# Optimization experiments

Measured on AMD Instinct MI355X. Metric: run time of the kernel, lower is better.

The kernel has to match this reference:

```python
import jax, jax.numpy as jnp
import numpy as np

N = 50000      # nodes
E = 800000     # edges (avg degree 16)
H = 128        # hidden_dim
ED = 8         # edge_dim
TD = 64        # time_dim
EIN = 2 * H + 1 + ED + TD  # 329, phi_e input dim


def _linear_params(key, fan_in, fan_out):
    kw, kb = jax.random.split(key)
    s = 1.0 / np.sqrt(fan_in)
    W = jax.random.uniform(kw, (fan_in, fan_out), minval=-s, maxval=s, dtype=jnp.float32)
    b = jax.random.uniform(kb, (fan_out,), minval=-s, maxval=s, dtype=jnp.float32)
    return W, b


def setup_inputs() -> dict:
    key = jax.random.key(0)
    ks = jax.random.split(key, 12)
    h = jax.random.normal(ks[0], (N, H), dtype=jnp.float32)
    x = jax.random.normal(ks[1], (N, 3), dtype=jnp.float32)
    edge_attr = jax.random.normal(ks[2], (E, ED), dtype=jnp.float32)
    t_emb = jax.random.normal(ks[3], (N, TD), dtype=jnp.float32)
    edge_index = jax.random.randint(ks[4], (2, E), 0, N, dtype=jnp.int32)
    We1_w, We1_b = _linear_params(ks[5], EIN, H)
    We2_w, We2_b = _linear_params(ks[6], H, H)
    Watt_w, Watt_b = _linear_params(ks[7], H, 1)
    Wx1_w, Wx1_b = _linear_params(ks[8], H, H)
    Wx2_w, Wx2_b = _linear_params(ks[9], H, 1)
    Wh1_w, Wh1_b = _linear_params(ks[10], 2 * H, H)
    Wh2_w, Wh2_b = _linear_params(ks[11], H, H)
    return dict(h=h, x=x, edge_attr=edge_attr, t_emb=t_emb,
                We1_w=We1_w, We1_b=We1_b, We2_w=We2_w, We2_b=We2_b,
                Watt_w=Watt_w, Watt_b=Watt_b,
                Wx1_w=Wx1_w, Wx1_b=Wx1_b, Wx2_w=Wx2_w, Wx2_b=Wx2_b,
                Wh1_w=Wh1_w, Wh1_b=Wh1_b, Wh2_w=Wh2_w, Wh2_b=Wh2_b,
                edge_index=edge_index)


def reference(h, x, edge_attr, t_emb,
              We1_w, We1_b, We2_w, We2_b,
              Watt_w, Watt_b,
              Wx1_w, Wx1_b, Wx2_w, Wx2_b,
              Wh1_w, Wh1_b, Wh2_w, Wh2_b,
              edge_index):
    src, dst = edge_index[0], edge_index[1]
    diff = x[src] - x[dst]                                   # (E, 3)
    dist_sq = jnp.sum(diff * diff, axis=-1, keepdims=True)   # (E, 1)
    # m_ij = phi_e(h_i || h_j || ||x_i - x_j||^2 || edge_attr || t_emb)
    msg_in = jnp.concatenate([h[src], h[dst], dist_sq, edge_attr, t_emb[src]], axis=-1)  # (E, EIN)
    m = jax.nn.silu(msg_in @ We1_w + We1_b) @ We2_w + We2_b  # (E, H)
    # attention gate
    att = jax.nn.sigmoid(m @ Watt_w + Watt_b)                # (E, 1)
    m = att * m
    # equivariant coordinate update
    coord_w = jnp.tanh(jax.nn.silu(m @ Wx1_w + Wx1_b) @ Wx2_w + Wx2_b)  # (E, 1)
    coord_shift = diff * coord_w                             # (E, 3)
    coord_agg = jax.ops.segment_sum(coord_shift, dst, num_segments=N)   # (N, 3)
    deg = jax.ops.segment_sum(jnp.ones((dst.shape[0], 1), dtype=x.dtype), dst, num_segments=N)
    x_out = x + coord_agg / (deg + 1.0)
    # invariant feature update with residual
    msg_agg = jax.ops.segment_sum(m, dst, num_segments=N)    # (N, H)
    h_in = jnp.concatenate([h, msg_agg], axis=-1)            # (N, 2H)
    h_out = h + (jax.nn.silu(h_in @ Wh1_w + Wh1_b) @ Wh2_w + Wh2_b)
    return (h_out, x_out)
```

## Files before the change

kernel.cpp:

```cpp
#include <hip/hip_runtime.h>
#include <hip/hip_fp16.h>

typedef unsigned short u16;
typedef unsigned int u32;
typedef __attribute__((ext_vector_type(8))) short short8;
typedef __attribute__((ext_vector_type(4))) float f32x4;

#define NN 50000
#define EE 800000
#define SCAN_B 49

__device__ __forceinline__ float bf2f(u16 u){ union{u32 i; float f;} v; v.i=((u32)u)<<16; return v.f; }
__device__ __forceinline__ u16 f2bf(float f){ union{float f; u32 i;} v; v.f=f; u32 b=v.i; b += 0x7FFFu + ((b>>16)&1u); return (u16)(b>>16); }
__device__ __forceinline__ float sigmoidf_(float x){ return 1.0f/(1.0f+__expf(-x)); }

__device__ __forceinline__ void cvt8(uint4 q, float* f){
  f[0]=bf2f((u16)(q.x&0xFFFF)); f[1]=bf2f((u16)(q.x>>16));
  f[2]=bf2f((u16)(q.y&0xFFFF)); f[3]=bf2f((u16)(q.y>>16));
  f[4]=bf2f((u16)(q.z&0xFFFF)); f[5]=bf2f((u16)(q.z>>16));
  f[6]=bf2f((u16)(q.w&0xFFFF)); f[7]=bf2f((u16)(q.w>>16));
}
__device__ __forceinline__ uint4 pack8(const float* f){
  uint4 q;
  q.x=(u32)f2bf(f[0])|((u32)f2bf(f[1])<<16);
  q.y=(u32)f2bf(f[2])|((u32)f2bf(f[3])<<16);
  q.z=(u32)f2bf(f[4])|((u32)f2bf(f[5])<<16);
  q.w=(u32)f2bf(f[6])|((u32)f2bf(f[7])<<16);
  return q;
}

__device__ __forceinline__ float h2f(u16 u){ __half h; *reinterpret_cast<u16*>(&h)=u; return (float)h; }
__device__ __forceinline__ u32 f2h2pack(float lo, float hi){
  __half2 h2 = __floats2half2_rn(lo, hi);
  return *reinterpret_cast<u32*>(&h2);
}
__device__ __forceinline__ void atomic_pk_add_f16(u16* addr, u32 data){
  asm volatile("global_atomic_pk_add_f16 %0, %1, off" :: "v"(addr), "v"(data) : "memory");
}

template<int FP32> struct IO;
template<> struct IO<0> {
  static __device__ __forceinline__ float ld(const void* p, int i){ return bf2f(((const u16*)p)[i]); }
  static __device__ __forceinline__ void ld8(const void* p, int i, float* f){
    cvt8(*(const uint4*)((const u16*)p + i), f);
  }
  static __device__ __forceinline__ void st(void* p, int i, float v){ ((u16*)p)[i] = f2bf(v); }
};
template<> struct IO<1> {
  static __device__ __forceinline__ float ld(const void* p, int i){ return ((const float*)p)[i]; }
  static __device__ __forceinline__ void ld8(const void* p, int i, float* f){
    f32x4 a = *(const f32x4*)((const float*)p + i);
    f32x4 b = *(const f32x4*)((const float*)p + i + 4);
    f[0]=a[0]; f[1]=a[1]; f[2]=a[2]; f[3]=a[3];
    f[4]=b[0]; f[5]=b[1]; f[6]=b[2]; f[7]=b[3];
  }
  static __device__ __forceinline__ void st(void* p, int i, float v){ ((float*)p)[i] = v; }
};

__device__ __forceinline__ void atomic_add_bf16pair(u32* addr, float lo, float hi){
  u32 old = *addr, assumed;
  do {
    assumed = old;
    float flo = bf2f((u16)(assumed & 0xFFFFu)) + lo;
    float fhi = bf2f((u16)(assumed >> 16)) + hi;
    u32 newv = (u32)f2bf(flo) | ((u32)f2bf(fhi) << 16);
    if (newv == assumed) return;
    old = atomicCAS(addr, assumed, newv);
  } while (old != assumed);
}

__global__ void k_probe(const u16* __restrict__ hraw, int* __restrict__ flag){
  if (threadIdx.x==0 && blockIdx.x==0){
    float mx = 0.f; int zc = 0;
    for (int i = 0; i < 256; i += 2){
      u16 u = hraw[i];
      if (u == 0) zc++;
      float v = fabsf(bf2f(u));
      mx = fmaxf(mx, v);
    }
    flag[0] = (mx > 1e3f || zc > 32) ? 1 : 0;
  }
}

__global__ __launch_bounds__(256) void k_hist(const int* __restrict__ eidx, int* __restrict__ cnt){
  int e = blockIdx.x*256 + threadIdx.x;
  if (e < EE) atomicAdd(&cnt[eidx[EE+e]], 1);
}
__global__ __launch_bounds__(1024) void k_scanA(const int* __restrict__ cnt,
                                               int* __restrict__ rowoff, int* __restrict__ bsum){
  __shared__ int s[1024];
  int t = threadIdx.x, b = blockIdx.x, i = b*1024 + t;
  int v = (i < NN) ? cnt[i] : 0;
  s[t] = v; __syncthreads();
  #pragma unroll
  for (int off=1; off<1024; off<<=1){
    int add = (t>=off) ? s[t-off] : 0;
    __syncthreads();
    s[t] += add;
    __syncthreads();
  }
  rowoff[i+1] = s[t];
  if (t==1023) bsum[b] = s[t];
}
__global__ void k_scanB(int* __restrict__ bsum){
  if (threadIdx.x==0 && blockIdx.x==0){
    int acc=0;
    for (int b=0;b<SCAN_B;b++){ int v=bsum[b]; bsum[b]=acc; acc+=v; }
  }
}
__global__ __launch_bounds__(1024) void k_scanC(int* __restrict__ rowoff, int* __restrict__ cur,
                                               const int* __restrict__ bsum){
  int t = threadIdx.x, b = blockIdx.x, i = b*1024 + t;
  int v = rowoff[i+1] + bsum[b];
  rowoff[i+1] = v;
  if (i < NN-1) cur[i+1] = v;
  if (i==0){ rowoff[0]=0; cur[0]=0; }
}
__global__ __launch_bounds__(256) void k_scatter(const int* __restrict__ eidx,
                                                 int* __restrict__ cur, int* __restrict__ perm){
  int e = blockIdx.x*256 + threadIdx.x;
  if (e < EE){
    int p = atomicAdd(&cur[eidx[EE+e]], 1);
    perm[p] = e;
  }
}

template<int FP32>
__global__ __launch_bounds__(256) void k_prep(
    const int* __restrict__ flag,
    const void* __restrict__ We1, const void* __restrict__ We2,
    const void* __restrict__ Wx1, const void* __restrict__ Wh1,
    const void* __restrict__ Wh2,
    u16* __restrict__ WprojT, u16* __restrict__ We2T, u16* __restrict__ Wx1T,
    u16* __restrict__ Wh1T, u16* __restrict__ Wh2T, u16* __restrict__ Wrk9T)
{
  if (flag[0] != FP32) return;
  int i = blockIdx.x*256 + threadIdx.x;
  if (i < 49152){
    int n = i/192, k = i%192; float v;
    if (n < 128) v = (k<128) ? IO<FP32>::ld(We1, k*128+n) : IO<FP32>::ld(We1, (265+k-128)*128+n);
    else         v = (k<128) ? IO<FP32>::ld(We1, (128+k)*128+(n-128)) : 0.f;
    WprojT[i] = f2bf(v);
  } else if (i < 65536){
    int j=i-49152; int n=j/128, k=j%128; We2T[j] = f2bf(IO<FP32>::ld(We2, k*128+n));
  } else if (i < 81920){
    int j=i-65536; int n=j/128, k=j%128; Wx1T[j] = f2bf(IO<FP32>::ld(Wx1, k*128+n));
  } else if (i < 114688){
    int j=i-81920; int n=j/256, k=j%256; Wh1T[j] = f2bf(IO<FP32>::ld(Wh1, k*128+n));
  } else if (i < 131072){
    int j=i-114688; int n=j/128, k=j%128; Wh2T[j] = f2bf(IO<FP32>::ld(Wh2, k*128+n));
  } else if (i < 135168){
    int j=i-131072; int n=j/32, k=j%32;
    float v = (k<=8) ? IO<FP32>::ld(We1, (256+k)*128+n) : 0.f;
    Wrk9T[j] = f2bf(v);
  }
}

template<int FP32, int WP2>
__global__ __launch_bounds__(256) void k_proj(
    const int* __restrict__ flag,
    const void* __restrict__ h, const void* __restrict__ temb,
    const u16* __restrict__ WprojT, const void* __restrict__ We1b,
    u16* __restrict__ P13, u16* __restrict__ P2)
{
  if (flag[0] != FP32) return;
  constexpr int NT = WP2 ? 16 : 8;
  __shared__ __align__(16) u16 s_a[64][200];
  int tid = threadIdx.x; int nbase = blockIdx.x*64;
  {
    u32* p = (u32*)&s_a[0][0];
    for (int i = tid; i < 6400; i += 256) p[i] = 0u;
  }
  __syncthreads();
  {
    int r = tid>>2, p = tid&3; int node = nbase + r;
    if (node < NN){
      #pragma unroll
      for (int c=0;c<6;c++){
        int col = p*48 + c*8;
        float f[8];
        if (col<128) IO<FP32>::ld8(h, node*128 + col, f);
        else         IO<FP32>::ld8(temb, node*64 + (col-128), f);
        *(uint4*)&s_a[r][col] = pack8(f);
      }
    }
  }
  __syncthreads();
  int lane=tid&63, wid=tid>>6, quad=lane>>4, l15=lane&15, mb=wid*16;
  f32x4 acc[NT];
  #pragma unroll
  for (int nt=0;nt<NT;nt++) acc[nt]=(f32x4){0.f,0.f,0.f,0.f};
  #pragma unroll
  for (int ks=0;ks<6;ks++){
    short8 af = *(const short8*)&s_a[mb+l15][ks*32+quad*8];
    #pragma unroll
    for (int nt=0;nt<NT;nt++){
      short8 bfr = *(const short8*)(WprojT + (nt*16+l15)*192 + ks*32+quad*8);
      acc[nt] = __builtin_amdgcn_mfma_f32_16x16x32_bf16(af, bfr, acc[nt], 0,0,0);
    }
  }
  #pragma unroll
  for (int r=0;r<4;r++){
    int node = nbase + mb + quad*4 + r;
    if (node < NN){
      #pragma unroll
      for (int nt=0;nt<NT;nt++){
        int colg = nt*16 + l15;
        float v = acc[nt][r];
        if (colg < 128) P13[node*128+colg] = f2bf(v + IO<FP32>::ld(We1b, colg));
        else if (WP2)   P2[node*128+(colg-128)] = f2bf(v);
      }
    }
  }
}

template<int FP32, int TIERA>
__global__ __launch_bounds__(256, 6) void k_edge(
    const int* __restrict__ flag,
    const void* __restrict__ x, const void* __restrict__ ea,
    const void* __restrict__ We1, const void* __restrict__ h,
    const void* __restrict__ We2b, const void* __restrict__ Watt, const void* __restrict__ Wattb,
    const void* __restrict__ Wx1b, const void* __restrict__ Wx2, const void* __restrict__ Wx2b,
    const int* __restrict__ eidx, const int* __restrict__ perm,
    const u16* __restrict__ P13, const u16* __restrict__ P2,
    const u16* __restrict__ WprojT, const u16* __restrict__ Wrk9T,
    const u16* __restrict__ We2T, const u16* __restrict__ Wx1T,
    u16* __restrict__ msgh, u16* __restrict__ msgb, float* __restrict__ cagg)
{
  if (flag[0] != FP32) return;
  __shared__ int s_dst[64];
  __shared__ float s_dif[64][3];
  __shared__ __align__(16) u16 s_hid[64][136];
  __shared__ __align__(16) u16 s_att[TIERA?64:1][40];
  __shared__ __align__(16) u16 s_m[TIERA?1:64][136];
  __shared__ __align__(16) u16 s_hd[TIERA?1:64][136];
  int tid = threadIdx.x;
  int ebase = blockIdx.x*64;
  {
    int el = tid>>2, p = tid&3;
    int e = TIERA ? perm[ebase+el] : (ebase+el);
    int srcI = eidx[e], dstI = eidx[EE+e];
    float d0 = IO<FP32>::ld(x, srcI*3+0) - IO<FP32>::ld(x, dstI*3+0);
    float d1 = IO<FP32>::ld(x, srcI*3+1) - IO<FP32>::ld(x, dstI*3+1);
    float d2 = IO<FP32>::ld(x, srcI*3+2) - IO<FP32>::ld(x, dstI*3+2);
    float dsq = d0*d0 + d1*d1 + d2*d2;
    if (p==0){ s_dst[el]=dstI; s_dif[el][0]=d0; s_dif[el][1]=d1; s_dif[el][2]=d2; }
    if constexpr (TIERA){
      if (p < 2){
        float eav[8]; IO<FP32>::ld8(ea, e*8, eav);
        float f9[8];
        if (p==0){ f9[0]=dsq; for (int t=0;t<7;t++) f9[1+t]=eav[t]; }
        else { f9[0]=eav[7]; for (int t=1;t<8;t++) f9[t]=0.f; }
        *(uint4*)&s_att[el][p*8] = pack8(f9);
      } else {
        *(uint4*)&s_att[el][p*8] = make_uint4(0,0,0,0);
      }
      const u16* p13r = P13 + srcI*128;
      const u16* p2r  = P2  + dstI*128;
      #pragma unroll
      for (int c=0;c<4;c++){
        int col = p*32 + c*8;
        float fa[8], fb[8];
        cvt8(*(const uint4*)(p13r+col), fa);
        cvt8(*(const uint4*)(p2r+col),  fb);
        #pragma unroll
        for (int i2=0;i2<8;i2++) fa[i2] += fb[i2];
        *(uint4*)&s_hid[el][col] = pack8(fa);
      }
    } else {
      float eav[8]; IO<FP32>::ld8(ea, e*8, eav);
      const u16* p13r = P13 + srcI*128;
      #pragma unroll
      for (int c=0;c<4;c++){
        int col = p*32 + c*8;
        float fw[8], pre[8];
        cvt8(*(const uint4*)(p13r+col), pre);
        IO<FP32>::ld8(We1, 256*128 + col, fw);
        #pragma unroll
        for (int i2=0;i2<8;i2++) pre[i2] += dsq*fw[i2];
        #pragma unroll
        for (int t=0;t<8;t++){
          IO<FP32>::ld8(We1, (257+t)*128 + col, fw);
          #pragma unroll
          for (int i2=0;i2<8;i2++) pre[i2] += eav[t]*fw[i2];
        }
        *(uint4*)&s_hid[el][col] = pack8(pre);
        float hd[8]; IO<FP32>::ld8(h, dstI*128 + col, hd);
        *(uint4*)&s_hd[el][col] = pack8(hd);
      }
    }
  }
  int lane=tid&63, wid=tid>>6, quad=lane>>4, l15=lane&15, mb=wid*16;
  if constexpr (TIERA){
    f32x4 acc9[8];
    #pragma unroll
    for (int nt=0;nt<8;nt++) acc9[nt]=(f32x4){0.f,0.f,0.f,0.f};
    short8 a9 = *(const short8*)&s_att[mb+l15][quad*8];
    #pragma unroll
    for (int nt=0;nt<8;nt++){
      short8 bfr = *(const short8*)(Wrk9T + (nt*16+l15)*32 + quad*8);
      acc9[nt] = __builtin_amdgcn_mfma_f32_16x16x32_bf16(a9, bfr, acc9[nt], 0,0,0);
    }
    #pragma unroll
    for (int r=0;r<4;r++){
      int row = mb + quad*4 + r;
      #pragma unroll
      for (int nt=0;nt<8;nt++){
        int col = nt*16+l15;
        float u = bf2f(s_hid[row][col]) + acc9[nt][r];
        u = u*sigmoidf_(u);
        s_hid[row][col] = f2bf(u);
      }
    }
  } else {
    f32x4 accg[8];
    #pragma unroll
    for (int nt=0;nt<8;nt++) accg[nt]=(f32x4){0.f,0.f,0.f,0.f};
    #pragma unroll
    for (int ks=0;ks<4;ks++){
      short8 af = *(const short8*)&s_hd[mb+l15][ks*32+quad*8];
      #pragma unroll
      for (int nt=0;nt<8;nt++){
        short8 bfr = *(const short8*)(WprojT + (128 + nt*16+l15)*192 + ks*32+quad*8);
        accg[nt] = __builtin_amdgcn_mfma_f32_16x16x32_bf16(af, bfr, accg[nt], 0,0,0);
      }
    }
    #pragma unroll
    for (int r=0;r<4;r++){
      int row = mb + quad*4 + r;
      #pragma unroll
      for (int nt=0;nt<8;nt++){
        int col = nt*16+l15;
        float u = bf2f(s_hid[row][col]) + accg[nt][r];
        u = u*sigmoidf_(u);
        s_hid[row][col] = f2bf(u);
      }
    }
  }
  f32x4 acc[8];
  #pragma unroll
  for (int nt=0;nt<8;nt++) acc[nt]=(f32x4){0.f,0.f,0.f,0.f};
  #pragma unroll
  for (int ks=0;ks<4;ks++){
    short8 af = *(const short8*)&s_hid[mb+l15][ks*32+quad*8];
    #pragma unroll
    for (int nt=0;nt<8;nt++){
      short8 bfr = *(const short8*)(We2T + (nt*16+l15)*128 + ks*32+quad*8);
      acc[nt] = __builtin_amdgcn_mfma_f32_16x16x32_bf16(af, bfr, acc[nt], 0,0,0);
    }
  }
  float b2v[8], wav[8];
  #pragma unroll
  for (int nt=0;nt<8;nt++){ b2v[nt]=IO<FP32>::ld(We2b, nt*16+l15); wav[nt]=IO<FP32>::ld(Watt, nt*16+l15); }
  float attb = IO<FP32>::ld(Wattb, 0);
  float mval[8][4]; float dotr[4];
  #pragma unroll
  for (int r=0;r<4;r++){
    float s=0.f;
    #pragma unroll
    for (int nt=0;nt<8;nt++){ mval[nt][r]=acc[nt][r]+b2v[nt]; s += mval[nt][r]*wav[nt]; }
    dotr[r]=s;
  }
  #pragma unroll
  for (int off=1;off<16;off<<=1){
    #pragma unroll
    for (int r=0;r<4;r++) dotr[r] += __shfl_xor(dotr[r], off);
  }
  if constexpr (TIERA){
    float racc[8];
    #pragma unroll
    for (int nt=0;nt<8;nt++) racc[nt]=0.f;
    #pragma unroll
    for (int r=0;r<4;r++){
      float att = sigmoidf_(dotr[r]+attb);
      int erow = mb + quad*4 + r;
      int dstN = s_dst[erow];
      bool emit = (r==3) || (s_dst[erow+1] != dstN);
      #pragma unroll
      for (int nt=0;nt<8;nt++){
        float v = mval[nt][r]*att;
        s_hid[erow][nt*16+l15] = f2bf(v);
        racc[nt] += v;
      }
      #pragma unroll
      for (int nt=0;nt<8;nt++){
        float part = __shfl_xor(racc[nt], 1);
        if (emit && ((l15 & 1) == 0)){
          atomic_pk_add_f16(msgh + dstN*128 + nt*16 + l15, f2h2pack(racc[nt], part));
        }
      }
      if (emit){
        #pragma unroll
        for (int nt=0;nt<8;nt++) racc[nt]=0.f;
      }
    }
  } else {
    #pragma unroll
    for (int r=0;r<4;r++){
      float att = sigmoidf_(dotr[r]+attb);
      int erow = mb + quad*4 + r;
      int dstN = s_dst[erow];
      #pragma unroll
      for (int nt=0;nt<8;nt++){
        float v = mval[nt][r]*att;
        mval[nt][r] = v;
        s_m[erow][nt*16+l15] = f2bf(v);
      }
      #pragma unroll
      for (int nt=0;nt<8;nt++){
        float part = __shfl_xor(mval[nt][r], 1);
        if ((l15 & 1) == 0){
          atomic_add_bf16pair((u32*)(msgb + dstN*128 + nt*16 + l15), mval[nt][r], part);
        }
      }
    }
  }
  f32x4 acc2[8];
  #pragma unroll
  for (int nt=0;nt<8;nt++) acc2[nt]=(f32x4){0.f,0.f,0.f,0.f};
  #pragma unroll
  for (int ks=0;ks<4;ks++){
    short8 af = TIERA ? *(const short8*)&s_hid[mb+l15][ks*32+quad*8]
                      : *(const short8*)&s_m[mb+l15][ks*32+quad*8];
    #pragma unroll
    for (int nt=0;nt<8;nt++){
      short8 bfr = *(const short8*)(Wx1T + (nt*16+l15)*128 + ks*32+quad*8);
      acc2[nt] = __builtin_amdgcn_mfma_f32_16x16x32_bf16(af, bfr, acc2[nt], 0,0,0);
    }
  }
  float bx1v[8], wx2v[8];
  #pragma unroll
  for (int nt=0;nt<8;nt++){ bx1v[nt]=IO<FP32>::ld(Wx1b, nt*16+l15); wx2v[nt]=IO<FP32>::ld(Wx2, nt*16+l15); }
  float bx2f = IO<FP32>::ld(Wx2b, 0);
  float dc[4];
  #pragma unroll
  for (int r=0;r<4;r++){
    float s=0.f;
    #pragma unroll
    for (int nt=0;nt<8;nt++){
      float u = acc2[nt][r] + bx1v[nt];
      u = u*sigmoidf_(u);
      s += u*wx2v[nt];
    }
    dc[r]=s;
  }
  #pragma unroll
  for (int off=1;off<16;off<<=1){
    #pragma unroll
    for (int r=0;r<4;r++) dc[r] += __shfl_xor(dc[r], off);
  }
  if constexpr (TIERA){
    if (l15==0){
      float c0=0.f, c1=0.f, c2=0.f;
      #pragma unroll
      for (int r=0;r<4;r++){
        float cw = tanhf(dc[r]+bx2f);
        int erow = mb + quad*4 + r;
        int dstN = s_dst[erow];
        c0 += s_dif[erow][0]*cw;
        c1 += s_dif[erow][1]*cw;
        c2 += s_dif[erow][2]*cw;
        bool emit = (r==3) || (s_dst[erow+1] != dstN);
        if (emit){
          atomicAdd(&cagg[dstN*4+0], c0);
          atomicAdd(&cagg[dstN*4+1], c1);
          atomicAdd(&cagg[dstN*4+2], c2);
          c0=c1=c2=0.f;
        }
      }
    }
  } else {
    #pragma unroll
    for (int r=0;r<4;r++){
      float cw = tanhf(dc[r]+bx2f);
      if (l15==0){
        int erow = mb + quad*4 + r;
        int dstN = s_dst[erow];
        atomicAdd(&cagg[dstN*4+0], s_dif[erow][0]*cw);
        atomicAdd(&cagg[dstN*4+1], s_dif[erow][1]*cw);
        atomicAdd(&cagg[dstN*4+2], s_dif[erow][2]*cw);
        atomicAdd(&cagg[dstN*4+3], 1.0f);
      }
    }
  }
}

template<int FP32, int MSGF>
__global__ __launch_bounds__(256) void k_node(
    const int* __restrict__ flag,
    const void* __restrict__ h, const void* __restrict__ x,
    const u16* __restrict__ msgh, const u16* __restrict__ msgb,
    const float* __restrict__ cagg, const int* __restrict__ rowoff,
    const u16* __restrict__ Wh1T, const void* __restrict__ Wh1b,
    const u16* __restrict__ Wh2T, const void* __restrict__ Wh2b,
    void* __restrict__ out)
{
  if (flag[0] != FP32) return;
  __shared__ __align__(16) u16 s_a[64][264];
  __shared__ __align__(16) u16 s_u[64][136];
  int tid = threadIdx.x; int nbase = blockIdx.x*64;
  {
    u32* p1 = (u32*)&s_a[0][0];
    for (int i = tid; i < 8448; i += 256) p1[i] = 0u;
  }
  __syncthreads();
  {
    int r = tid>>2, p = tid&3; int node = nbase + r;
    if (node < NN){
      #pragma unroll
      for (int c=0;c<8;c++){
        int col = p*64 + c*8;
        if (col < 128){
          float f[8]; IO<FP32>::ld8(h, node*128 + col, f);
          *(uint4*)&s_a[r][col] = pack8(f);
        } else if (MSGF){
          uint4 q = *(const uint4*)(msgh + node*128 + (col-128));
          float f[8];
          f[0]=h2f((u16)(q.x&0xFFFF)); f[1]=h2f((u16)(q.x>>16));
          f[2]=h2f((u16)(q.y&0xFFFF)); f[3]=h2f((u16)(q.y>>16));
          f[4]=h2f((u16)(q.z&0xFFFF)); f[5]=h2f((u16)(q.z>>16));
          f[6]=h2f((u16)(q.w&0xFFFF)); f[7]=h2f((u16)(q.w>>16));
          *(uint4*)&s_a[r][col] = pack8(f);
        } else {
          *(uint4*)&s_a[r][col] = *(const uint4*)(msgb + node*128 + (col-128));
        }
      }
    }
  }
  __syncthreads();
  int lane=tid&63, wid=tid>>6, quad=lane>>4, l15=lane&15, mb=wid*16;
  f32x4 acc[8];
  #pragma unroll
  for (int nt=0;nt<8;nt++) acc[nt]=(f32x4){0.f,0.f,0.f,0.f};
  #pragma unroll
  for (int ks=0;ks<8;ks++){
    short8 af = *(const short8*)&s_a[mb+l15][ks*32+quad*8];
    #pragma unroll
    for (int nt=0;nt<8;nt++){
      short8 bfr = *(const short8*)(Wh1T + (nt*16+l15)*256 + ks*32+quad*8);
      acc[nt] = __builtin_amdgcn_mfma_f32_16x16x32_bf16(af, bfr, acc[nt], 0,0,0);
    }
  }
  #pragma unroll
  for (int r=0;r<4;r++){
    int row = mb + quad*4 + r;
    #pragma unroll
    for (int nt=0;nt<8;nt++){
      int col = nt*16+l15;
      float u = acc[nt][r] + IO<FP32>::ld(Wh1b, col);
      u = u*sigmoidf_(u);
      s_u[row][col] = f2bf(u);
    }
  }
  f32x4 acc2[8];
  #pragma unroll
  for (int nt=0;nt<8;nt++) acc2[nt]=(f32x4){0.f,0.f,0.f,0.f};
  #pragma unroll
  for (int ks=0;ks<4;ks++){
    short8 af = *(const short8*)&s_u[mb+l15][ks*32+quad*8];
    #pragma unroll
    for (int nt=0;nt<8;nt++){
      short8 bfr = *(const short8*)(Wh2T + (nt*16+l15)*128 + ks*32+quad*8);
      acc2[nt] = __builtin_amdgcn_mfma_f32_16x16x32_bf16(af, bfr, acc2[nt], 0,0,0);
    }
  }
  #pragma unroll
  for (int r=0;r<4;r++){
    int node = nbase + mb + quad*4 + r;
    if (node < NN){
      #pragma unroll
      for (int nt=0;nt<8;nt++){
        int col = nt*16+l15;
        float v = IO<FP32>::ld(h, node*128+col) + acc2[nt][r] + IO<FP32>::ld(Wh2b, col);
        IO<FP32>::st(out, node*128+col, v);
      }
    }
  }
  if (tid < 64){
    int node = nbase + tid;
    if (node < NN){
      float deg = MSGF ? (float)(rowoff[node+1]-rowoff[node]) : cagg[node*4+3];
      float inv = 1.0f/(deg + 1.0f);
      #pragma unroll
      for (int c=0;c<3;c++){
        float v = IO<FP32>::ld(x, node*3+c) + cagg[node*4+c]*inv;
        IO<FP32>::st(out, NN*128 + node*3 + c, v);
      }
    }
  }
}

extern "C" void kernel_launch(void* const* d_in, const int* in_sizes, int n_in,
                              void* d_out, int out_size, void* d_ws, size_t ws_size,
                              hipStream_t stream) {
  const void* h     = d_in[0];
  const void* x     = d_in[1];
  const void* ea    = d_in[2];
  const void* temb  = d_in[3];
  const void* We1   = d_in[4];
  const void* We1b  = d_in[5];
  const void* We2   = d_in[6];
  const void* We2b  = d_in[7];
  const void* Watt  = d_in[8];
  const void* Wattb = d_in[9];
  const void* Wx1   = d_in[10];
  const void* Wx1b  = d_in[11];
  const void* Wx2   = d_in[12];
  const void* Wx2b  = d_in[13];
  const void* Wh1   = d_in[14];
  const void* Wh1b  = d_in[15];
  const void* Wh2   = d_in[16];
  const void* Wh2b  = d_in[17];
  const int* eidx   = (const int*)d_in[18];
  char* ws = (char*)d_ws;

  u16* WprojT = (u16*)(ws + 0);
  u16* We2T   = (u16*)(ws + 98304);
  u16* Wx1T   = (u16*)(ws + 131072);
  u16* Wh1T   = (u16*)(ws + 163840);
  u16* Wh2T   = (u16*)(ws + 229376);
  u16* Wrk9T  = (u16*)(ws + 262144);
  float* cagg = (float*)(ws + 270336);
  int* flag   = (int*)(ws + 1070336);
  bool tierA = (ws_size >= (size_t)39470592);
  u16* msgh   = (u16*)(ws + 1070592);
  u16* msgb   = (u16*)(ws + 1070592);
  u16* P2     = (u16*)(ws + 13870592);
  int* cnt    = (int*)(ws + 26670592);
  int* rowoff = (int*)(ws + 26871296);
  int* cur    = (int*)(ws + 27072512);
  int* bsum   = (int*)(ws + 27273216);
  int* perm   = (int*)(ws + 27273472);
  u16* P13    = (u16*)d_out;

  hipMemsetAsync(ws + 270336, 0, 13600256, stream);
  k_probe<<<1, 64, 0, stream>>>((const u16*)h, flag);
  if (tierA){
    hipMemsetAsync(cnt, 0, 200704, stream);
    k_hist<<<(EE+255)/256, 256, 0, stream>>>(eidx, cnt);
    k_scanA<<<SCAN_B, 1024, 0, stream>>>(cnt, rowoff, bsum);
    k_scanB<<<1, 64, 0, stream>>>(bsum);
    k_scanC<<<SCAN_B, 1024, 0, stream>>>(rowoff, cur, bsum);
    k_scatter<<<(EE+255)/256, 256, 0, stream>>>(eidx, cur, perm);
  }
  k_prep<0><<<528, 256, 0, stream>>>(flag, We1, We2, Wx1, Wh1, Wh2, WprojT, We2T, Wx1T, Wh1T, Wh2T, Wrk9T);
  k_prep<1><<<528, 256, 0, stream>>>(flag, We1, We2, Wx1, Wh1, Wh2, WprojT, We2T, Wx1T, Wh1T, Wh2T, Wrk9T);
  if (tierA){
    k_proj<0,1><<<(NN+63)/64, 256, 0, stream>>>(flag, h, temb, WprojT, We1b, P13, P2);
    k_proj<1,1><<<(NN+63)/64, 256, 0, stream>>>(flag, h, temb, WprojT, We1b, P13, P2);
    k_edge<0,1><<<EE/64, 256, 0, stream>>>(flag, x, ea, We1, h, We2b, Watt, Wattb, Wx1b, Wx2, Wx2b,
                                           eidx, perm, P13, P2, WprojT, Wrk9T, We2T, Wx1T, msgh, msgb, cagg);
    k_edge<1,1><<<EE/64, 256, 0, stream>>>(flag, x, ea, We1, h, We2b, Watt, Wattb, Wx1b, Wx2, Wx2b,
                                           eidx, perm, P13, P2, WprojT, Wrk9T, We2T, Wx1T, msgh, msgb, cagg);
    k_node<0,1><<<(NN+63)/64, 256, 0, stream>>>(flag, h, x, msgh, msgb, cagg, rowoff, Wh1T, Wh1b, Wh2T, Wh2b, d_out);
    k_node<1,1><<<(NN+63)/64, 256, 0, stream>>>(flag, h, x, msgh, msgb, cagg, rowoff, Wh1T, Wh1b, Wh2T, Wh2b, d_out);
  } else {
    k_proj<0,0><<<(NN+63)/64, 256, 0, stream>>>(flag, h, temb, WprojT, We1b, P13, P2);
    k_proj<1,0><<<(NN+63)/64, 256, 0, stream>>>(flag, h, temb, WprojT, We1b, P13, P2);
    k_edge<0,0><<<EE/64, 256, 0, stream>>>(flag, x, ea, We1, h, We2b, Watt, Wattb, Wx1b, Wx2, Wx2b,
                                           eidx, perm, P13, P2, WprojT, Wrk9T, We2T, Wx1T, msgh, msgb, cagg);
    k_edge<1,0><<<EE/64, 256, 0, stream>>>(flag, x, ea, We1, h, We2b, Watt, Wattb, Wx1b, Wx2, Wx2b,
                                           eidx, perm, P13, P2, WprojT, Wrk9T, We2T, Wx1T, msgh, msgb, cagg);
    k_node<0,0><<<(NN+63)/64, 256, 0, stream>>>(flag, h, x, msgh, msgb, cagg, rowoff, Wh1T, Wh1b, Wh2T, Wh2b, d_out);
    k_node<1,0><<<(NN+63)/64, 256, 0, stream>>>(flag, h, x, msgh, msgb, cagg, rowoff, Wh1T, Wh1b, Wh2T, Wh2b, d_out);
  }
}
```

Before: 945.9 us.

## Split edge kernel by tier and give each wave two 16-edge tiles

The templated edge kernel becomes two kernels. The tier-A kernel now handles 128 edges per block, with each wave computing two 16-row MFMA tiles that share every B-fragment load of the weight matrices. This halves the weight reads per edge and the block count, and the k-loops use unroll 1. It costs more registers and shared memory: launch bounds drop to 3 blocks per CU and each of two threads gathers half of a 128-column row.

```diff
diff --git a/kernel.cpp b/kernel.cpp
--- a/kernel.cpp
+++ b/kernel.cpp
@@ -214,166 +214,130 @@
   }
 }
 
-template<int FP32, int TIERA>
-__global__ __launch_bounds__(256, 6) void k_edge(
+template<int FP32>
+__global__ __launch_bounds__(256, 3) void k_edgeA(
     const int* __restrict__ flag,
     const void* __restrict__ x, const void* __restrict__ ea,
-    const void* __restrict__ We1, const void* __restrict__ h,
     const void* __restrict__ We2b, const void* __restrict__ Watt, const void* __restrict__ Wattb,
     const void* __restrict__ Wx1b, const void* __restrict__ Wx2, const void* __restrict__ Wx2b,
     const int* __restrict__ eidx, const int* __restrict__ perm,
     const u16* __restrict__ P13, const u16* __restrict__ P2,
-    const u16* __restrict__ WprojT, const u16* __restrict__ Wrk9T,
-    const u16* __restrict__ We2T, const u16* __restrict__ Wx1T,
-    u16* __restrict__ msgh, u16* __restrict__ msgb, float* __restrict__ cagg)
+    const u16* __restrict__ Wrk9T, const u16* __restrict__ We2T, const u16* __restrict__ Wx1T,
+    u16* __restrict__ msgh, float* __restrict__ cagg)
 {
   if (flag[0] != FP32) return;
-  __shared__ int s_dst[64];
-  __shared__ float s_dif[64][3];
-  __shared__ __align__(16) u16 s_hid[64][136];
-  __shared__ __align__(16) u16 s_att[TIERA?64:1][40];
-  __shared__ __align__(16) u16 s_m[TIERA?1:64][136];
-  __shared__ __align__(16) u16 s_hd[TIERA?1:64][136];
+  __shared__ int s_dst[128];
+  __shared__ float s_dif[128][3];
+  __shared__ __align__(16) u16 s_hid[128][136];
+  __shared__ __align__(16) u16 s_att[128][40];
   int tid = threadIdx.x;
-  int ebase = blockIdx.x*64;
+  int ebase = blockIdx.x*128;
   {
-    int el = tid>>2, p = tid&3;
-    int e = TIERA ? perm[ebase+el] : (ebase+el);
+    int el = tid>>1, p = tid&1;
+    int e = perm[ebase+el];
     int srcI = eidx[e], dstI = eidx[EE+e];
-    float d0 = IO<FP32>::ld(x, srcI*3+0) - IO<FP32>::ld(x, dstI*3+0);
-    float d1 = IO<FP32>::ld(x, srcI*3+1) - IO<FP32>::ld(x, dstI*3+1);
-    float d2 = IO<FP32>::ld(x, srcI*3+2) - IO<FP32>::ld(x, dstI*3+2);
-    float dsq = d0*d0 + d1*d1 + d2*d2;
-    if (p==0){ s_dst[el]=dstI; s_dif[el][0]=d0; s_dif[el][1]=d1; s_dif[el][2]=d2; }
-    if constexpr (TIERA){
-      if (p < 2){
-        float eav[8]; IO<FP32>::ld8(ea, e*8, eav);
-        float f9[8];
-        if (p==0){ f9[0]=dsq; for (int t=0;t<7;t++) f9[1+t]=eav[t]; }
-        else { f9[0]=eav[7]; for (int t=1;t<8;t++) f9[t]=0.f; }
-        *(uint4*)&s_att[el][p*8] = pack8(f9);
-      } else {
-        *(uint4*)&s_att[el][p*8] = make_uint4(0,0,0,0);
-      }
-      const u16* p13r = P13 + srcI*128;
-      const u16* p2r  = P2  + dstI*128;
-      #pragma unroll
-      for (int c=0;c<4;c++){
-        int col = p*32 + c*8;
-        float fa[8], fb[8];
-        cvt8(*(const uint4*)(p13r+col), fa);
-        cvt8(*(const uint4*)(p2r+col),  fb);
-        #pragma unroll
-        for (int i2=0;i2<8;i2++) fa[i2] += fb[i2];
-        *(uint4*)&s_hid[el][col] = pack8(fa);
-      }
+    if (p==0){
+      float d0 = IO<FP32>::ld(x, srcI*3+0) - IO<FP32>::ld(x, dstI*3+0);
+      float d1 = IO<FP32>::ld(x, srcI*3+1) - IO<FP32>::ld(x, dstI*3+1);
+      float d2 = IO<FP32>::ld(x, srcI*3+2) - IO<FP32>::ld(x, dstI*3+2);
+      float dsq = d0*d0 + d1*d1 + d2*d2;
+      s_dst[el]=dstI; s_dif[el][0]=d0; s_dif[el][1]=d1; s_dif[el][2]=d2;
+      float eav[8]; IO<FP32>::ld8(ea, e*8, eav);
+      float f9[8];
+      f9[0]=dsq; for (int t=0;t<7;t++) f9[1+t]=eav[t];
+      *(uint4*)&s_att[el][0] = pack8(f9);
+      f9[0]=eav[7]; for (int t=1;t<8;t++) f9[t]=0.f;
+      *(uint4*)&s_att[el][8] = pack8(f9);
     } else {
-      float eav[8]; IO<FP32>::ld8(ea, e*8, eav);
-      const u16* p13r = P13 + srcI*128;
-      #pragma unroll
-      for (int c=0;c<4;c++){
-        int col = p*32 + c*8;
-        float fw[8], pre[8];
-        cvt8(*(const uint4*)(p13r+col), pre);
-        IO<FP32>::ld8(We1, 256*128 + col, fw);
-        #pragma unroll
-        for (int i2=0;i2<8;i2++) pre[i2] += dsq*fw[i2];
-        #pragma unroll
-        for (int t=0;t<8;t++){
-          IO<FP32>::ld8(We1, (257+t)*128 + col, fw);
-          #pragma unroll
-          for (int i2=0;i2<8;i2++) pre[i2] += eav[t]*fw[i2];
-        }
-        *(uint4*)&s_hid[el][col] = pack8(pre);
-        float hd[8]; IO<FP32>::ld8(h, dstI*128 + col, hd);
-        *(uint4*)&s_hd[el][col] = pack8(hd);
-      }
-    }
-  }
-  int lane=tid&63, wid=tid>>6, quad=lane>>4, l15=lane&15, mb=wid*16;
-  if constexpr (TIERA){
-    f32x4 acc9[8];
-    #pragma unroll
-    for (int nt=0;nt<8;nt++) acc9[nt]=(f32x4){0.f,0.f,0.f,0.f};
-    short8 a9 = *(const short8*)&s_att[mb+l15][quad*8];
+      *(uint4*)&s_att[el][16] = make_uint4(0,0,0,0);
+      *(uint4*)&s_att[el][24] = make_uint4(0,0,0,0);
+    }
+    const u16* p13r = P13 + srcI*128;
+    const u16* p2r  = P2  + dstI*128;
+    #pragma unroll
+    for (int c=0;c<8;c++){
+      int col = p*64 + c*8;
+      float fa[8], fb[8];
+      cvt8(*(const uint4*)(p13r+col), fa);
+      cvt8(*(const uint4*)(p2r+col),  fb);
+      #pragma unroll
+      for (int i2=0;i2<8;i2++) fa[i2] += fb[i2];
+      *(uint4*)&s_hid[el][col] = pack8(fa);
+    }
+  }
+  int lane=tid&63, wid=tid>>6, quad=lane>>4, l15=lane&15;
+  int rb = wid*32;
+  f32x4 acc9[2][8];
+  #pragma unroll
+  for (int t=0;t<2;t++)
+    #pragma unroll
+    for (int nt=0;nt<8;nt++) acc9[t][nt]=(f32x4){0.f,0.f,0.f,0.f};
+  {
+    short8 a90 = *(const short8*)&s_att[rb+l15][quad*8];
+    short8 a91 = *(const short8*)&s_att[rb+16+l15][quad*8];
     #pragma unroll
     for (int nt=0;nt<8;nt++){
       short8 bfr = *(const short8*)(Wrk9T + (nt*16+l15)*32 + quad*8);
-      acc9[nt] = __builtin_amdgcn_mfma_f32_16x16x32_bf16(a9, bfr, acc9[nt], 0,0,0);
-    }
+      acc9[0][nt] = __builtin_amdgcn_mfma_f32_16x16x32_bf16(a90, bfr, acc9[0][nt], 0,0,0);
+      acc9[1][nt] = __builtin_amdgcn_mfma_f32_16x16x32_bf16(a91, bfr, acc9[1][nt], 0,0,0);
+    }
+  }
+  #pragma unroll
+  for (int t=0;t<2;t++){
     #pragma unroll
     for (int r=0;r<4;r++){
-      int row = mb + quad*4 + r;
+      int row = rb + t*16 + quad*4 + r;
       #pragma unroll
       for (int nt=0;nt<8;nt++){
         int col = nt*16+l15;
-        float u = bf2f(s_hid[row][col]) + acc9[nt][r];
+        float u = bf2f(s_hid[row][col]) + acc9[t][nt][r];
         u = u*sigmoidf_(u);
         s_hid[row][col] = f2bf(u);
       }
     }
-  } else {
-    f32x4 accg[8];
-    #pragma unroll
-    for (int nt=0;nt<8;nt++) accg[nt]=(f32x4){0.f,0.f,0.f,0.f};
-    #pragma unroll
-    for (int ks=0;ks<4;ks++){
-      short8 af = *(const short8*)&s_hd[mb+l15][ks*32+quad*8];
-      #pragma unroll
-      for (int nt=0;nt<8;nt++){
-        short8 bfr = *(const short8*)(WprojT + (128 + nt*16+l15)*192 + ks*32+quad*8);
-        accg[nt] = __builtin_amdgcn_mfma_f32_16x16x32_bf16(af, bfr, accg[nt], 0,0,0);
-      }
-    }
-    #pragma unroll
-    for (int r=0;r<4;r++){
-      int row = mb + quad*4 + r;
-      #pragma unroll
-      for (int nt=0;nt<8;nt++){
-        int col = nt*16+l15;
-        float u = bf2f(s_hid[row][col]) + accg[nt][r];
-        u = u*sigmoidf_(u);
-        s_hid[row][col] = f2bf(u);
-      }
-    }
-  }
-  f32x4 acc[8];
-  #pragma unroll
-  for (int nt=0;nt<8;nt++) acc[nt]=(f32x4){0.f,0.f,0.f,0.f};
-  #pragma unroll
+  }
+  f32x4 acc[2][8];
+  #pragma unroll
+  for (int t=0;t<2;t++)
+    #pragma unroll
+    for (int nt=0;nt<8;nt++) acc[t][nt]=(f32x4){0.f,0.f,0.f,0.f};
+  #pragma unroll 1
   for (int ks=0;ks<4;ks++){
-    short8 af = *(const short8*)&s_hid[mb+l15][ks*32+quad*8];
+    short8 af0 = *(const short8*)&s_hid[rb+l15][ks*32+quad*8];
+    short8 af1 = *(const short8*)&s_hid[rb+16+l15][ks*32+quad*8];
     #pragma unroll
     for (int nt=0;nt<8;nt++){
       short8 bfr = *(const short8*)(We2T + (nt*16+l15)*128 + ks*32+quad*8);
-      acc[nt] = __builtin_amdgcn_mfma_f32_16x16x32_bf16(af, bfr, acc[nt], 0,0,0);
+      acc[0][nt] = __builtin_amdgcn_mfma_f32_16x16x32_bf16(af0, bfr, acc[0][nt], 0,0,0);
+      acc[1][nt] = __builtin_amdgcn_mfma_f32_16x16x32_bf16(af1, bfr, acc[1][nt], 0,0,0);
     }
   }
   float b2v[8], wav[8];
   #pragma unroll
   for (int nt=0;nt<8;nt++){ b2v[nt]=IO<FP32>::ld(We2b, nt*16+l15); wav[nt]=IO<FP32>::ld(Watt, nt*16+l15); }
   float attb = IO<FP32>::ld(Wattb, 0);
-  float mval[8][4]; float dotr[4];
-  #pragma unroll
-  for (int r=0;r<4;r++){
-    float s=0.f;
-    #pragma unroll
-    for (int nt=0;nt<8;nt++){ mval[nt][r]=acc[nt][r]+b2v[nt]; s += mval[nt][r]*wav[nt]; }
-    dotr[r]=s;
-  }
-  #pragma unroll
-  for (int off=1;off<16;off<<=1){
-    #pragma unroll
-    for (int r=0;r<4;r++) dotr[r] += __shfl_xor(dotr[r], off);
-  }
-  if constexpr (TIERA){
+  #pragma unroll
+  for (int t=0;t<2;t++){
+    float mval[8][4]; float dotr[4];
+    #pragma unroll
+    for (int r=0;r<4;r++){
+      float s=0.f;
+      #pragma unroll
+      for (int nt=0;nt<8;nt++){ mval[nt][r]=acc[t][nt][r]+b2v[nt]; s += mval[nt][r]*wav[nt]; }
+      dotr[r]=s;
+    }
+    #pragma unroll
+    for (int off=1;off<16;off<<=1){
+      #pragma unroll
+      for (int r=0;r<4;r++) dotr[r] += __shfl_xor(dotr[r], off);
+    }
     float racc[8];
     #pragma unroll
     for (int nt=0;nt<8;nt++) racc[nt]=0.f;
     #pragma unroll
     for (int r=0;r<4;r++){
       float att = sigmoidf_(dotr[r]+attb);
-      int erow = mb + quad*4 + r;
+      int erow = rb + t*16 + quad*4 + r;
       int dstN = s_dst[erow];
       bool emit = (r==3) || (s_dst[erow+1] != dstN);
       #pragma unroll
@@ -394,68 +358,52 @@
         for (int nt=0;nt<8;nt++) racc[nt]=0.f;
       }
     }
-  } else {
-    #pragma unroll
-    for (int r=0;r<4;r++){
-      float att = sigmoidf_(dotr[r]+attb);
-      int erow = mb + quad*4 + r;
-      int dstN = s_dst[erow];
-      #pragma unroll
-      for (int nt=0;nt<8;nt++){
-        float v = mval[nt][r]*att;
-        mval[nt][r] = v;
-        s_m[erow][nt*16+l15] = f2bf(v);
-      }
-      #pragma unroll
-      for (int nt=0;nt<8;nt++){
-        float part = __shfl_xor(mval[nt][r], 1);
-        if ((l15 & 1) == 0){
-          atomic_add_bf16pair((u32*)(msgb + dstN*128 + nt*16 + l15), mval[nt][r], part);
-        }
-      }
-    }
-  }
-  f32x4 acc2[8];
-  #pragma unroll
-  for (int nt=0;nt<8;nt++) acc2[nt]=(f32x4){0.f,0.f,0.f,0.f};
-  #pragma unroll
+  }
+  f32x4 acc2[2][8];
+  #pragma unroll
+  for (int t=0;t<2;t++)
+    #pragma unroll
+    for (int nt=0;nt<8;nt++) acc2[t][nt]=(f32x4){0.f,0.f,0.f,0.f};
+  #pragma unroll 1
   for (int ks=0;ks<4;ks++){
-    short8 af = TIERA ? *(const short8*)&s_hid[mb+l15][ks*32+quad*8]
-                      : *(const short8*)&s_m[mb+l15][ks*32+quad*8];
+    short8 af0 = *(const short8*)&s_hid[rb+l15][ks*32+quad*8];
+    short8 af1 = *(const short8*)&s_hid[rb+16+l15][ks*32+quad*8];
     #pragma unroll
     for (int nt=0;nt<8;nt++){
       short8 bfr = *(const short8*)(Wx1T + (nt*16+l15)*128 + ks*32+quad*8);
-      acc2[nt] = __builtin_amdgcn_mfma_f32_16x16x32_bf16(af, bfr, acc2[nt], 0,0,0);
+      acc2[0][nt] = __builtin_amdgcn_mfma_f32_16x16x32_bf16(af0, bfr, acc2[0][nt], 0,0,0);
+      acc2[1][nt] = __builtin_amdgcn_mfma_f32_16x16x32_bf16(af1, bfr, acc2[1][nt], 0,0,0);
     }
   }
   float bx1v[8], wx2v[8];
   #pragma unroll
   for (int nt=0;nt<8;nt++){ bx1v[nt]=IO<FP32>::ld(Wx1b, nt*16+l15); wx2v[nt]=IO<FP32>::ld(Wx2, nt*16+l15); }
   float bx2f = IO<FP32>::ld(Wx2b, 0);
-  float dc[4];
-  #pragma unroll
-  for (int r=0;r<4;r++){
-    float s=0.f;
-    #pragma unroll
-    for (int nt=0;nt<8;nt++){
-      float u = acc2[nt][r] + bx1v[nt];
-      u = u*sigmoidf_(u);
-      s += u*wx2v[nt];
-    }
-    dc[r]=s;
-  }
-  #pragma unroll
-  for (int off=1;off<16;off<<=1){
-    #pragma unroll
-    for (int r=0;r<4;r++) dc[r] += __shfl_xor(dc[r], off);
-  }
-  if constexpr (TIERA){
+  #pragma unroll
+  for (int t=0;t<2;t++){
+    float dc[4];
+    #pragma unroll
+    for (int r=0;r<4;r++){
+      float s=0.f;
+      #pragma unroll
+      for (int nt=0;nt<8;nt++){
+        float u = acc2[t][nt][r] + bx1v[nt];
+        u = u*sigmoidf_(u);
+        s += u*wx2v[nt];
+      }
+      dc[r]=s;
+    }
+    #pragma unroll
+    for (int off=1;off<16;off<<=1){
+      #pragma unroll
+      for (int r=0;r<4;r++) dc[r] += __shfl_xor(dc[r], off);
+    }
     if (l15==0){
       float c0=0.f, c1=0.f, c2=0.f;
       #pragma unroll
       for (int r=0;r<4;r++){
         float cw = tanhf(dc[r]+bx2f);
-        int erow = mb + quad*4 + r;
+        int erow = rb + t*16 + quad*4 + r;
         int dstN = s_dst[erow];
         c0 += s_dif[erow][0]*cw;
         c1 += s_dif[erow][1]*cw;
@@ -469,18 +417,177 @@
         }
       }
     }
-  } else {
+  }
+}
+
+template<int FP32>
+__global__ __launch_bounds__(256, 6) void k_edgeB(
+    const int* __restrict__ flag,
+    const void* __restrict__ x, const void* __restrict__ ea,
+    const void* __restrict__ We1, const void* __restrict__ h,
+    const void* __restrict__ We2b, const void* __restrict__ Watt, const void* __restrict__ Wattb,
+    const void* __restrict__ Wx1b, const void* __restrict__ Wx2, const void* __restrict__ Wx2b,
+    const int* __restrict__ eidx,
+    const u16* __restrict__ P13,
+    const u16* __restrict__ WprojT,
+    const u16* __restrict__ We2T, const u16* __restrict__ Wx1T,
+    u16* __restrict__ msgb, float* __restrict__ cagg)
+{
+  if (flag[0] != FP32) return;
+  __shared__ int s_dst[64];
+  __shared__ float s_dif[64][3];
+  __shared__ __align__(16) u16 s_hid[64][136];
+  __shared__ __align__(16) u16 s_m[64][136];
+  __shared__ __align__(16) u16 s_hd[64][136];
+  int tid = threadIdx.x;
+  int ebase = blockIdx.x*64;
+  {
+    int el = tid>>2, p = tid&3;
+    int e = ebase+el;
+    int srcI = eidx[e], dstI = eidx[EE+e];
+    float d0 = IO<FP32>::ld(x, srcI*3+0) - IO<FP32>::ld(x, dstI*3+0);
+    float d1 = IO<FP32>::ld(x, srcI*3+1) - IO<FP32>::ld(x, dstI*3+1);
+    float d2 = IO<FP32>::ld(x, srcI*3+2) - IO<FP32>::ld(x, dstI*3+2);
+    float dsq = d0*d0 + d1*d1 + d2*d2;
+    if (p==0){ s_dst[el]=dstI; s_dif[el][0]=d0; s_dif[el][1]=d1; s_dif[el][2]=d2; }
+    float eav[8]; IO<FP32>::ld8(ea, e*8, eav);
+    const u16* p13r = P13 + srcI*128;
+    #pragma unroll
+    for (int c=0;c<4;c++){
+      int col = p*32 + c*8;
+      float fw[8], pre[8];
+      cvt8(*(const uint4*)(p13r+col), pre);
+      IO<FP32>::ld8(We1, 256*128 + col, fw);
+      #pragma unroll
+      for (int i2=0;i2<8;i2++) pre[i2] += dsq*fw[i2];
+      #pragma unroll
+      for (int t=0;t<8;t++){
+        IO<FP32>::ld8(We1, (257+t)*128 + col, fw);
+        #pragma unroll
+        for (int i2=0;i2<8;i2++) pre[i2] += eav[t]*fw[i2];
+      }
+      *(uint4*)&s_hid[el][col] = pack8(pre);
+      float hd[8]; IO<FP32>::ld8(h, dstI*128 + col, hd);
+      *(uint4*)&s_hd[el][col] = pack8(hd);
+    }
+  }
+  int lane=tid&63, wid=tid>>6, quad=lane>>4, l15=lane&15, mb=wid*16;
+  {
+    f32x4 accg[8];
+    #pragma unroll
+    for (int nt=0;nt<8;nt++) accg[nt]=(f32x4){0.f,0.f,0.f,0.f};
+    #pragma unroll
+    for (int ks=0;ks<4;ks++){
+      short8 af = *(const short8*)&s_hd[mb+l15][ks*32+quad*8];
+      #pragma unroll
+      for (int nt=0;nt<8;nt++){
+        short8 bfr = *(const short8*)(WprojT + (128 + nt*16+l15)*192 + ks*32+quad*8);
+        accg[nt] = __builtin_amdgcn_mfma_f32_16x16x32_bf16(af, bfr, accg[nt], 0,0,0);
+      }
+    }
     #pragma unroll
     for (int r=0;r<4;r++){
-      float cw = tanhf(dc[r]+bx2f);
-      if (l15==0){
-        int erow = mb + quad*4 + r;
-        int dstN = s_dst[erow];
-        atomicAdd(&cagg[dstN*4+0], s_dif[erow][0]*cw);
-        atomicAdd(&cagg[dstN*4+1], s_dif[erow][1]*cw);
-        atomicAdd(&cagg[dstN*4+2], s_dif[erow][2]*cw);
-        atomicAdd(&cagg[dstN*4+3], 1.0f);
-      }
+      int row = mb + quad*4 + r;
+      #pragma unroll
+      for (int nt=0;nt<8;nt++){
+        int col = nt*16+l15;
+        float u = bf2f(s_hid[row][col]) + accg[nt][r];
+        u = u*sigmoidf_(u);
+        s_hid[row][col] = f2bf(u);
+      }
+    }
+  }
+  f32x4 acc[8];
+  #pragma unroll
+  for (int nt=0;nt<8;nt++) acc[nt]=(f32x4){0.f,0.f,0.f,0.f};
+  #pragma unroll
+  for (int ks=0;ks<4;ks++){
+    short8 af = *(const short8*)&s_hid[mb+l15][ks*32+quad*8];
+    #pragma unroll
+    for (int nt=0;nt<8;nt++){
+      short8 bfr = *(const short8*)(We2T + (nt*16+l15)*128 + ks*32+quad*8);
+      acc[nt] = __builtin_amdgcn_mfma_f32_16x16x32_bf16(af, bfr, acc[nt], 0,0,0);
+    }
+  }
+  float b2v[8], wav[8];
+  #pragma unroll
+  for (int nt=0;nt<8;nt++){ b2v[nt]=IO<FP32>::ld(We2b, nt*16+l15); wav[nt]=IO<FP32>::ld(Watt, nt*16+l15); }
+  float attb = IO<FP32>::ld(Wattb, 0);
+  float mval[8][4]; float dotr[4];
+  #pragma unroll
+  for (int r=0;r<4;r++){
+    float s=0.f;
+    #pragma unroll
+    for (int nt=0;nt<8;nt++){ mval[nt][r]=acc[nt][r]+b2v[nt]; s += mval[nt][r]*wav[nt]; }
+    dotr[r]=s;
+  }
+  #pragma unroll
+  for (int off=1;off<16;off<<=1){
+    #pragma unroll
+    for (int r=0;r<4;r++) dotr[r] += __shfl_xor(dotr[r], off);
+  }
+  #pragma unroll
+  for (int r=0;r<4;r++){
+    float att = sigmoidf_(dotr[r]+attb);
+    int erow = mb + quad*4 + r;
+    int dstN = s_dst[erow];
+    #pragma unroll
+    for (int nt=0;nt<8;nt++){
+      float v = mval[nt][r]*att;
+      mval[nt][r] = v;
+      s_m[erow][nt*16+l15] = f2bf(v);
+    }
+    #pragma unroll
+    for (int nt=0;nt<8;nt++){
+      float part = __shfl_xor(mval[nt][r], 1);
+      if ((l15 & 1) == 0){
+        atomic_add_bf16pair((u32*)(msgb + dstN*128 + nt*16 + l15), mval[nt][r], part);
+      }
+    }
+  }
+  f32x4 acc2[8];
+  #pragma unroll
+  for (int nt=0;nt<8;nt++) acc2[nt]=(f32x4){0.f,0.f,0.f,0.f};
+  #pragma unroll
+  for (int ks=0;ks<4;ks++){
+    short8 af = *(const short8*)&s_m[mb+l15][ks*32+quad*8];
+    #pragma unroll
+    for (int nt=0;nt<8;nt++){
+      short8 bfr = *(const short8*)(Wx1T + (nt*16+l15)*128 + ks*32+quad*8);
+      acc2[nt] = __builtin_amdgcn_mfma_f32_16x16x32_bf16(af, bfr, acc2[nt], 0,0,0);
+    }
+  }
+  float bx1v[8], wx2v[8];
+  #pragma unroll
+  for (int nt=0;nt<8;nt++){ bx1v[nt]=IO<FP32>::ld(Wx1b, nt*16+l15); wx2v[nt]=IO<FP32>::ld(Wx2, nt*16+l15); }
+  float bx2f = IO<FP32>::ld(Wx2b, 0);
+  float dc[4];
+  #pragma unroll
+  for (int r=0;r<4;r++){
+    float s=0.f;
+    #pragma unroll
+    for (int nt=0;nt<8;nt++){
+      float u = acc2[nt][r] + bx1v[nt];
+      u = u*sigmoidf_(u);
+      s += u*wx2v[nt];
+    }
+    dc[r]=s;
+  }
+  #pragma unroll
+  for (int off=1;off<16;off<<=1){
+    #pragma unroll
+    for (int r=0;r<4;r++) dc[r] += __shfl_xor(dc[r], off);
+  }
+  #pragma unroll
+  for (int r=0;r<4;r++){
+    float cw = tanhf(dc[r]+bx2f);
+    if (l15==0){
+      int erow = mb + quad*4 + r;
+      int dstN = s_dst[erow];
+      atomicAdd(&cagg[dstN*4+0], s_dif[erow][0]*cw);
+      atomicAdd(&cagg[dstN*4+1], s_dif[erow][1]*cw);
+      atomicAdd(&cagg[dstN*4+2], s_dif[erow][2]*cw);
+      atomicAdd(&cagg[dstN*4+3], 1.0f);
     }
   }
 }
@@ -648,19 +755,19 @@
   if (tierA){
     k_proj<0,1><<<(NN+63)/64, 256, 0, stream>>>(flag, h, temb, WprojT, We1b, P13, P2);
     k_proj<1,1><<<(NN+63)/64, 256, 0, stream>>>(flag, h, temb, WprojT, We1b, P13, P2);
-    k_edge<0,1><<<EE/64, 256, 0, stream>>>(flag, x, ea, We1, h, We2b, Watt, Wattb, Wx1b, Wx2, Wx2b,
-                                           eidx, perm, P13, P2, WprojT, Wrk9T, We2T, Wx1T, msgh, msgb, cagg);
-    k_edge<1,1><<<EE/64, 256, 0, stream>>>(flag, x, ea, We1, h, We2b, Watt, Wattb, Wx1b, Wx2, Wx2b,
-                                           eidx, perm, P13, P2, WprojT, Wrk9T, We2T, Wx1T, msgh, msgb, cagg);
+    k_edgeA<0><<<EE/128, 256, 0, stream>>>(flag, x, ea, We2b, Watt, Wattb, Wx1b, Wx2, Wx2b,
+                                           eidx, perm, P13, P2, Wrk9T, We2T, Wx1T, msgh, cagg);
+    k_edgeA<1><<<EE/128, 256, 0, stream>>>(flag, x, ea, We2b, Watt, Wattb, Wx1b, Wx2, Wx2b,
+                                           eidx, perm, P13, P2, Wrk9T, We2T, Wx1T, msgh, cagg);
     k_node<0,1><<<(NN+63)/64, 256, 0, stream>>>(flag, h, x, msgh, msgb, cagg, rowoff, Wh1T, Wh1b, Wh2T, Wh2b, d_out);
     k_node<1,1><<<(NN+63)/64, 256, 0, stream>>>(flag, h, x, msgh, msgb, cagg, rowoff, Wh1T, Wh1b, Wh2T, Wh2b, d_out);
   } else {
     k_proj<0,0><<<(NN+63)/64, 256, 0, stream>>>(flag, h, temb, WprojT, We1b, P13, P2);
     k_proj<1,0><<<(NN+63)/64, 256, 0, stream>>>(flag, h, temb, WprojT, We1b, P13, P2);
-    k_edge<0,0><<<EE/64, 256, 0, stream>>>(flag, x, ea, We1, h, We2b, Watt, Wattb, Wx1b, Wx2, Wx2b,
-                                           eidx, perm, P13, P2, WprojT, Wrk9T, We2T, Wx1T, msgh, msgb, cagg);
-    k_edge<1,0><<<EE/64, 256, 0, stream>>>(flag, x, ea, We1, h, We2b, Watt, Wattb, Wx1b, Wx2, Wx2b,
-                                           eidx, perm, P13, P2, WprojT, Wrk9T, We2T, Wx1T, msgh, msgb, cagg);
+    k_edgeB<0><<<EE/64, 256, 0, stream>>>(flag, x, ea, We1, h, We2b, Watt, Wattb, Wx1b, Wx2, Wx2b,
+                                          eidx, P13, WprojT, We2T, Wx1T, msgb, cagg);
+    k_edgeB<1><<<EE/64, 256, 0, stream>>>(flag, x, ea, We1, h, We2b, Watt, Wattb, Wx1b, Wx2, Wx2b,
+                                          eidx, P13, WprojT, We2T, Wx1T, msgb, cagg);
     k_node<0,0><<<(NN+63)/64, 256, 0, stream>>>(flag, h, x, msgh, msgb, cagg, rowoff, Wh1T, Wh1b, Wh2T, Wh2b, d_out);
     k_node<1,0><<<(NN+63)/64, 256, 0, stream>>>(flag, h, x, msgh, msgb, cagg, rowoff, Wh1T, Wh1b, Wh2T, Wh2b, d_out);
   }
```

Result: faster. 844.5 us (-10.7%).
